# Kernel optimization log

Hardware: AMD Instinct MI355X
Metric: run time of the kernel (lower is better)

## Reference

```python
import jax, jax.numpy as jnp
import numpy as np

H = 1024
L = 2

def setup_inputs() -> dict:
    key = jax.random.key(0)
    k1, k2, k3, k4, k5 = jax.random.split(key, 5)
    B, S = 32, 2048
    scale = 1.0 / np.sqrt(H)
    return {
        "query": jax.random.normal(k1, (B, 1, H * L), dtype=jnp.float32),
        "keys": jax.random.normal(k2, (B, S, H), dtype=jnp.float32),
        "Wa_w": jax.random.normal(k3, (H * L, H), dtype=jnp.float32) * scale,
        "Wa_b": jnp.zeros((H,), dtype=jnp.float32),
        "Ua_w": jax.random.normal(k4, (H, H), dtype=jnp.float32) * scale,
        "Ua_b": jnp.zeros((H,), dtype=jnp.float32),
        "Va_w": jax.random.normal(k5, (H, 1), dtype=jnp.float32) * scale,
        "Va_b": jnp.zeros((1,), dtype=jnp.float32),
    }

def reference(query, keys, Wa_w, Wa_b, Ua_w, Ua_b, Va_w, Va_b):
    # query: [B,1,H*L], keys: [B,S,H]
    q = jnp.einsum('bqd,dh->bqh', query, Wa_w) + Wa_b   # [B,1,H]
    k = jnp.einsum('bsd,dh->bsh', keys, Ua_w) + Ua_b    # [B,S,H]
    e = jnp.tanh(q + k)                                  # [B,S,H]
    scores = jnp.einsum('bsh,ho->bso', e, Va_w) + Va_b   # [B,S,1]
    scores = scores[:, :, 0][:, None, :]                 # [B,1,S]
    weights = jax.nn.softmax(scores, axis=-1)            # [B,1,S]
    context = jnp.einsum('bqs,bsh->bqh', weights, keys)  # [B,1,H]
    return (context, weights)
```

## Files before the change

kernel.cpp:

```cpp
#include <hip/hip_runtime.h>
#include <hip/hip_bf16.h>


typedef __attribute__((ext_vector_type(8))) short short8;
typedef __attribute__((ext_vector_type(4))) float floatx4;

typedef const __attribute__((address_space(1))) unsigned int gu32;
typedef __attribute__((address_space(3))) unsigned int lu32;

__device__ __forceinline__ unsigned short f2bf(float f) {
    union { float f; unsigned int u; } c; c.f = f;
    unsigned int u = c.u + 0x7fffu + ((c.u >> 16) & 1u);
    return (unsigned short)(u >> 16);
}

__device__ __forceinline__ unsigned int f2bf2(float lo, float hi) {
#if __has_builtin(__builtin_amdgcn_cvt_pk_bf16_f32)
    auto r = __builtin_amdgcn_cvt_pk_bf16_f32(lo, hi);
    unsigned int u; __builtin_memcpy(&u, &r, 4);
    return u;
#else
    return (unsigned int)f2bf(lo) | ((unsigned int)f2bf(hi) << 16);
#endif
}

__device__ __forceinline__ void gld16(const unsigned short* g, unsigned short* l) {
    __builtin_amdgcn_global_load_lds(
        (gu32*)(uintptr_t)g,
        (lu32*)(unsigned int)(uintptr_t)l,
        16, 0, 0);
}

__global__ __launch_bounds__(256) void qproj_k(
    const float* __restrict__ query, const float* __restrict__ Wa,
    const float* __restrict__ Wab, const float* __restrict__ Uab,
    float* __restrict__ qws)
{
    __shared__ float qs[2048];
    __shared__ float red[16*64];
    const int tid = threadIdx.x;
    const int b = blockIdx.x, hc = blockIdx.y;
    #pragma unroll
    for (int i = 0; i < 8; i++) qs[tid + 256*i] = query[b*2048 + tid + 256*i];
    __syncthreads();
    const int hq = tid & 15;
    const int dg = tid >> 4;
    const float4* wp = reinterpret_cast<const float4*>(Wa + (size_t)(dg*128)*1024 + hc*64 + hq*4);
    const float* qp = qs + dg*128;
    float4 a0; a0.x = a0.y = a0.z = a0.w = 0.f;
    float4 a1; a1.x = a1.y = a1.z = a1.w = 0.f;
    #pragma unroll 4
    for (int d = 0; d < 128; d += 2) {
        float q0 = qp[d], q1 = qp[d+1];
        float4 w0 = wp[(size_t)d*256];
        float4 w1 = wp[(size_t)(d+1)*256];
        a0.x += q0*w0.x; a0.y += q0*w0.y; a0.z += q0*w0.z; a0.w += q0*w0.w;
        a1.x += q1*w1.x; a1.y += q1*w1.y; a1.z += q1*w1.z; a1.w += q1*w1.w;
    }
    a0.x += a1.x; a0.y += a1.y; a0.z += a1.z; a0.w += a1.w;
    *reinterpret_cast<float4*>(red + dg*64 + hq*4) = a0;
    __syncthreads();
    if (tid < 64) {
        float v = 0.f;
        #pragma unroll
        for (int g = 0; g < 16; g++) v += red[g*64 + tid];
        int hh = hc*64 + tid;
        qws[b*1024 + hh] = v + Wab[hh] + Uab[hh];
    }
}

__global__ __launch_bounds__(256) void uat_k(const float* __restrict__ Ua,
                                             unsigned short* __restrict__ uat)
{
    __shared__ unsigned short t[64][65];
    const int x = threadIdx.x & 63, yy = threadIdx.x >> 6;
    const int d0 = blockIdx.x*64, h0 = blockIdx.y*64;
    #pragma unroll
    for (int i = 0; i < 16; i++) {
        int y = yy*16 + i;
        t[y][x] = f2bf(Ua[(size_t)(d0+y)*1024 + h0 + x]);
    }
    __syncthreads();
    #pragma unroll
    for (int i = 0; i < 16; i++) {
        int y = yy*16 + i;
        uat[(size_t)(h0+y)*1024 + d0 + x] = t[x][y];
    }
}

__global__ __launch_bounds__(256) void kb16_k(const float* __restrict__ keys,
                                              unsigned short* __restrict__ kb,
                                              unsigned int nf4)
{
    const unsigned int stride = gridDim.x * 256u;
    unsigned int f = blockIdx.x * 256u + threadIdx.x;
    #pragma unroll 4
    for (int it = 0; it < 4; ++it, f += stride) {
        if (f < nf4) {
            unsigned int elem = f << 2;
            unsigned int rg   = elem >> 10;
            unsigned int rem  = elem & 1023u;
            unsigned int g    = rem >> 5;
            unsigned int c    = (rem >> 3) & 3u;
            unsigned int half = (rem >> 2) & 1u;
            unsigned int p    = ((rg & 2047u) >> 1) & 3u;
            float4 v = reinterpret_cast<const float4*>(keys)[f];
            uint2 w;
            w.x = f2bf2(v.x, v.y);
            w.y = f2bf2(v.z, v.w);
            unsigned int dst = rg*1024u + g*32u + ((c ^ p) << 3) + (half << 2);
            *reinterpret_cast<uint2*>(kb + dst) = w;
        }
    }
}

__global__ __launch_bounds__(256) void score_gemm_fast(
    const unsigned short* __restrict__ kb16,
    const unsigned short* __restrict__ uat,
    const float* __restrict__ qws,
    const float* __restrict__ Va,
    float* __restrict__ score,
    int b0)
{
    __shared__ unsigned short aS[2][128*32];
    __shared__ unsigned short bS[2][128*32];
    const int tid = threadIdx.x;
    const int bz = blockIdx.z;
    const int b = b0 + bz;
    const int s0 = blockIdx.x * 128;
    const int h0 = blockIdx.y * 128;
    const int lane = tid & 63, wave = tid >> 6;
    const int quad = lane >> 4, l15 = lane & 15;
    const int wm = (wave & 1) * 64, wn = (wave >> 1) * 64;

    const int srow = lane >> 2;
    const int schunk = (lane & 3) ^ ((srow >> 1) & 3);
    const int c0 = wave*2, c1 = wave*2 + 1;
    const unsigned short* ubase = uat + (size_t)h0*1024;
    const size_t boff0 = (size_t)(c0*16 + srow)*1024 + schunk*8;
    const size_t boff1 = (size_t)(c1*16 + srow)*1024 + schunk*8;

    const unsigned short* kA = kb16 + (size_t)(bz*2048 + s0)*1024;
    const size_t aoff0 = (size_t)(tid >> 2)*1024 + (size_t)(tid & 3)*8;
    const size_t aoff1 = (size_t)(64 + (tid >> 2))*1024 + (size_t)(tid & 3)*8;

    floatx4 acc[4][4];
    #pragma unroll
    for (int i = 0; i < 4; i++)
        #pragma unroll
        for (int j = 0; j < 4; j++) acc[i][j] = (floatx4)0.0f;

    gld16(kA + aoff0,    aS[0] + wave*512);
    gld16(kA + aoff1,    aS[0] + 2048 + wave*512);
    gld16(ubase + boff0, bS[0] + c0*512);
    gld16(ubase + boff1, bS[0] + c1*512);
    __syncthreads();

    int cur = 0;
    for (int kt = 0; kt < 31; ++kt) {
        const int nxt = cur ^ 1;
        const int k1 = (kt + 1) << 5;

        gld16(kA + aoff0 + k1,    aS[nxt] + wave*512);
        gld16(kA + aoff1 + k1,    aS[nxt] + 2048 + wave*512);
        gld16(ubase + boff0 + k1, bS[nxt] + c0*512);
        gld16(ubase + boff1 + k1, bS[nxt] + c1*512);

        short8 af[4], bf8[4];
        #pragma unroll
        for (int i = 0; i < 4; i++) {
            int row = wm + 16*i + l15;
            af[i] = *reinterpret_cast<const short8*>(aS[cur] + row*32 + ((quad ^ ((row>>1)&3)) * 8));
        }
        #pragma unroll
        for (int j = 0; j < 4; j++) {
            int row = wn + 16*j + l15;
            bf8[j] = *reinterpret_cast<const short8*>(bS[cur] + row*32 + ((quad ^ ((row>>1)&3)) * 8));
        }
        #pragma unroll
        for (int i = 0; i < 4; i++)
            #pragma unroll
            for (int j = 0; j < 4; j++)
                acc[i][j] = __builtin_amdgcn_mfma_f32_16x16x32_bf16(af[i], bf8[j], acc[i][j], 0, 0, 0);

        __syncthreads();
        cur = nxt;
    }

    {
        short8 af[4], bf8[4];
        #pragma unroll
        for (int i = 0; i < 4; i++) {
            int row = wm + 16*i + l15;
            af[i] = *reinterpret_cast<const short8*>(aS[cur] + row*32 + ((quad ^ ((row>>1)&3)) * 8));
        }
        #pragma unroll
        for (int j = 0; j < 4; j++) {
            int row = wn + 16*j + l15;
            bf8[j] = *reinterpret_cast<const short8*>(bS[cur] + row*32 + ((quad ^ ((row>>1)&3)) * 8));
        }
        #pragma unroll
        for (int i = 0; i < 4; i++)
            #pragma unroll
            for (int j = 0; j < 4; j++)
                acc[i][j] = __builtin_amdgcn_mfma_f32_16x16x32_bf16(af[i], bf8[j], acc[i][j], 0, 0, 0);
    }

    float qv[4], vav[4];
    #pragma unroll
    for (int j = 0; j < 4; j++) {
        int n = h0 + wn + 16*j + l15;
        qv[j]  = qws[b*1024 + n];
        vav[j] = Va[n];
    }
    #pragma unroll
    for (int i = 0; i < 4; i++) {
        #pragma unroll
        for (int r = 0; r < 4; r++) {
            float p = 0.f;
            #pragma unroll
            for (int j = 0; j < 4; j++) {
                float x = qv[j] + acc[i][j][r];
                float e = __expf(2.f * x);
                float t = 1.f - 2.f * __builtin_amdgcn_rcpf(e + 1.f);
                p += vav[j] * t;
            }
            #pragma unroll
            for (int off = 1; off < 16; off <<= 1) p += __shfl_xor(p, off, 64);
            if (l15 == 0) {
                int m = wm + 16*i + quad*4 + r;
                atomicAdd(score + (size_t)b*2048 + s0 + m, p);
            }
        }
    }
}

__global__ __launch_bounds__(256) void softmax_k(const float* __restrict__ score,
                                                 float* __restrict__ out_w)
{
    const int tid = threadIdx.x;
    const int b = blockIdx.x;
    __shared__ float wred[4], wred2[4];
    float sc[8];
    float mx = -3.0e38f;
    #pragma unroll
    for (int i = 0; i < 8; i++) {
        sc[i] = score[(size_t)b*2048 + tid + 256*i];
        mx = fmaxf(mx, sc[i]);
    }
    #pragma unroll
    for (int off = 32; off >= 1; off >>= 1) mx = fmaxf(mx, __shfl_xor(mx, off, 64));
    if ((tid & 63) == 0) wred[tid >> 6] = mx;
    __syncthreads();
    mx = fmaxf(fmaxf(wred[0], wred[1]), fmaxf(wred[2], wred[3]));
    float e[8]; float lsum = 0.f;
    #pragma unroll
    for (int i = 0; i < 8; i++) { e[i] = __expf(sc[i] - mx); lsum += e[i]; }
    #pragma unroll
    for (int off = 32; off >= 1; off >>= 1) lsum += __shfl_xor(lsum, off, 64);
    if ((tid & 63) == 0) wred2[tid >> 6] = lsum;
    __syncthreads();
    float inv = 1.0f / (wred2[0] + wred2[1] + wred2[2] + wred2[3]);
    #pragma unroll
    for (int i = 0; i < 8; i++) out_w[b*2048 + tid + 256*i] = e[i] * inv;
}

__global__ __launch_bounds__(256) void ctx_k(const float* __restrict__ keys,
                                             const float* __restrict__ w,
                                             float* __restrict__ ctxp, int sper)
{
    const int tid = threadIdx.x;
    const int b = blockIdx.x, sc = blockIdx.y;
    const float4* k4 = reinterpret_cast<const float4*>(keys) + (size_t)(b*2048 + sc*sper)*256;
    const float* wp = w + b*2048 + sc*sper;
    float4 a; a.x = a.y = a.z = a.w = 0.f;
    #pragma unroll 4
    for (int s = 0; s < sper; s++) {
        float wv = wp[s];
        float4 kv = k4[(size_t)s*256 + tid];
        a.x += wv*kv.x; a.y += wv*kv.y; a.z += wv*kv.z; a.w += wv*kv.w;
    }
    reinterpret_cast<float4*>(ctxp)[((size_t)b*gridDim.y + sc)*256 + tid] = a;
}

__global__ __launch_bounds__(256) void ctxsum_k(const float* __restrict__ ctxp,
                                                float* __restrict__ out, int nc)
{
    const int idx = blockIdx.x*256 + threadIdx.x;
    const int b = idx >> 10, h = idx & 1023;
    float v = 0.f;
    for (int s = 0; s < nc; s++) v += ctxp[((size_t)b*nc + s)*1024 + h];
    out[idx] = v;
}

extern "C" void kernel_launch(void* const* d_in, const int* in_sizes, int n_in,
                              void* d_out, int out_size, void* d_ws, size_t ws_size,
                              hipStream_t stream)
{
    const float* query = (const float*)d_in[0];
    const float* keys  = (const float*)d_in[1];
    const float* Wa_w  = (const float*)d_in[2];
    const float* Wa_b  = (const float*)d_in[3];
    const float* Ua_w  = (const float*)d_in[4];
    const float* Ua_b  = (const float*)d_in[5];
    const float* Va_w  = (const float*)d_in[6];

    char* ws = (char*)d_ws;
    float*          qws     = (float*)(ws);
    unsigned short* uat     = (unsigned short*)(ws + (131072));
    float*          score   = (float*)(ws + (131072 + 2097152));
    float*          ctxp    = (float*)(ws + (131072 + 2097152 + 4194304));
    const size_t BASE = 131072 + 2097152 + 4194304 + 2097152;
    unsigned short* kb16 = (unsigned short*)(ws + BASE);

    size_t avail = (ws_size > BASE) ? (ws_size - BASE) : 0;
    int nb = 32;
    while (nb > 1 && (size_t)nb * 2048 * 1024 * 2 > avail) nb >>= 1;

    float* out_ctx = (float*)d_out;
    float* out_w   = out_ctx + 32*1024;

    hipMemsetAsync(score, 0, 32*2048*sizeof(float), stream);
    qproj_k<<<dim3(32, 16), 256, 0, stream>>>(query, Wa_w, Wa_b, Ua_b, qws);
    uat_k  <<<dim3(16, 16), 256, 0, stream>>>(Ua_w, uat);
    for (int b0 = 0; b0 < 32; b0 += nb) {
        unsigned int nf4 = (unsigned int)nb * 2048u * 256u;
        unsigned int nthr = (nf4 + 3u) / 4u;
        unsigned int nblk = (nthr + 255u) / 256u;
        kb16_k<<<dim3(nblk), 256, 0, stream>>>(keys + (size_t)b0*2048*1024, kb16, nf4);
        score_gemm_fast<<<dim3(16, 8, nb), 256, 0, stream>>>(kb16, uat, qws, Va_w, score, b0);
    }
    softmax_k<<<dim3(32),      256, 0, stream>>>(score, out_w);
    ctx_k    <<<dim3(32, 16),  256, 0, stream>>>(keys, out_w, ctxp, 128);
    ctxsum_k <<<dim3(128),     256, 0, stream>>>(ctxp, out_ctx, 16);
}
```

Before: 647.4 us.

## Widen score GEMM tile to 128x256 and fuse context reduction via atomics

The score GEMM block tile grows from 128x128 to 128x256 along H. Each wave now computes 64x128 with 32 accumulators, which halves the B-tile loads and the atomic score writes per output and improves reuse of the A tile in LDS. Separately, the context partial-sum kernel is removed, and ctx_k atomically adds its partials straight into the zeroed output. The trade-offs are higher register pressure (128 accumulator floats per thread), more LDS, half as many blocks (lower occupancy and parallelism), and nondeterministic float atomics.

New measurement: 622.4 us. 3.9% less time.

```diff
diff --git a/kernel.cpp b/kernel.cpp
--- a/kernel.cpp
+++ b/kernel.cpp
@@ -123,37 +123,41 @@
     int b0)
 {
     __shared__ unsigned short aS[2][128*32];
-    __shared__ unsigned short bS[2][128*32];
+    __shared__ unsigned short bS[2][256*32];
     const int tid = threadIdx.x;
     const int bz = blockIdx.z;
     const int b = b0 + bz;
     const int s0 = blockIdx.x * 128;
-    const int h0 = blockIdx.y * 128;
+    const int h0 = blockIdx.y * 256;
     const int lane = tid & 63, wave = tid >> 6;
     const int quad = lane >> 4, l15 = lane & 15;
-    const int wm = (wave & 1) * 64, wn = (wave >> 1) * 64;
+    const int wm = (wave & 1) * 64, wn = (wave >> 1) * 128;
 
     const int srow = lane >> 2;
     const int schunk = (lane & 3) ^ ((srow >> 1) & 3);
-    const int c0 = wave*2, c1 = wave*2 + 1;
     const unsigned short* ubase = uat + (size_t)h0*1024;
-    const size_t boff0 = (size_t)(c0*16 + srow)*1024 + schunk*8;
-    const size_t boff1 = (size_t)(c1*16 + srow)*1024 + schunk*8;
+    size_t boff[4];
+    #pragma unroll
+    for (int u = 0; u < 4; u++) {
+        int cg = wave*4 + u;
+        boff[u] = (size_t)(cg*16 + srow)*1024 + schunk*8;
+    }
 
     const unsigned short* kA = kb16 + (size_t)(bz*2048 + s0)*1024;
     const size_t aoff0 = (size_t)(tid >> 2)*1024 + (size_t)(tid & 3)*8;
     const size_t aoff1 = (size_t)(64 + (tid >> 2))*1024 + (size_t)(tid & 3)*8;
 
-    floatx4 acc[4][4];
+    floatx4 acc[4][8];
     #pragma unroll
     for (int i = 0; i < 4; i++)
         #pragma unroll
-        for (int j = 0; j < 4; j++) acc[i][j] = (floatx4)0.0f;
-
-    gld16(kA + aoff0,    aS[0] + wave*512);
-    gld16(kA + aoff1,    aS[0] + 2048 + wave*512);
-    gld16(ubase + boff0, bS[0] + c0*512);
-    gld16(ubase + boff1, bS[0] + c1*512);
+        for (int j = 0; j < 8; j++) acc[i][j] = (floatx4)0.0f;
+
+    gld16(kA + aoff0, aS[0] + wave*512);
+    gld16(kA + aoff1, aS[0] + 2048 + wave*512);
+    #pragma unroll
+    for (int u = 0; u < 4; u++)
+        gld16(ubase + boff[u], bS[0] + (wave*4 + u)*512);
     __syncthreads();
 
     int cur = 0;
@@ -161,26 +165,27 @@
         const int nxt = cur ^ 1;
         const int k1 = (kt + 1) << 5;
 
-        gld16(kA + aoff0 + k1,    aS[nxt] + wave*512);
-        gld16(kA + aoff1 + k1,    aS[nxt] + 2048 + wave*512);
-        gld16(ubase + boff0 + k1, bS[nxt] + c0*512);
-        gld16(ubase + boff1 + k1, bS[nxt] + c1*512);
-
-        short8 af[4], bf8[4];
+        gld16(kA + aoff0 + k1, aS[nxt] + wave*512);
+        gld16(kA + aoff1 + k1, aS[nxt] + 2048 + wave*512);
+        #pragma unroll
+        for (int u = 0; u < 4; u++)
+            gld16(ubase + boff[u] + k1, bS[nxt] + (wave*4 + u)*512);
+
+        short8 af[4], bf8[8];
         #pragma unroll
         for (int i = 0; i < 4; i++) {
             int row = wm + 16*i + l15;
             af[i] = *reinterpret_cast<const short8*>(aS[cur] + row*32 + ((quad ^ ((row>>1)&3)) * 8));
         }
         #pragma unroll
-        for (int j = 0; j < 4; j++) {
+        for (int j = 0; j < 8; j++) {
             int row = wn + 16*j + l15;
             bf8[j] = *reinterpret_cast<const short8*>(bS[cur] + row*32 + ((quad ^ ((row>>1)&3)) * 8));
         }
         #pragma unroll
         for (int i = 0; i < 4; i++)
             #pragma unroll
-            for (int j = 0; j < 4; j++)
+            for (int j = 0; j < 8; j++)
                 acc[i][j] = __builtin_amdgcn_mfma_f32_16x16x32_bf16(af[i], bf8[j], acc[i][j], 0, 0, 0);
 
         __syncthreads();
@@ -188,27 +193,27 @@
     }
 
     {
-        short8 af[4], bf8[4];
+        short8 af[4], bf8[8];
         #pragma unroll
         for (int i = 0; i < 4; i++) {
             int row = wm + 16*i + l15;
             af[i] = *reinterpret_cast<const short8*>(aS[cur] + row*32 + ((quad ^ ((row>>1)&3)) * 8));
         }
         #pragma unroll
-        for (int j = 0; j < 4; j++) {
+        for (int j = 0; j < 8; j++) {
             int row = wn + 16*j + l15;
             bf8[j] = *reinterpret_cast<const short8*>(bS[cur] + row*32 + ((quad ^ ((row>>1)&3)) * 8));
         }
         #pragma unroll
         for (int i = 0; i < 4; i++)
             #pragma unroll
-            for (int j = 0; j < 4; j++)
+            for (int j = 0; j < 8; j++)
                 acc[i][j] = __builtin_amdgcn_mfma_f32_16x16x32_bf16(af[i], bf8[j], acc[i][j], 0, 0, 0);
     }
 
-    float qv[4], vav[4];
-    #pragma unroll
-    for (int j = 0; j < 4; j++) {
+    float qv[8], vav[8];
+    #pragma unroll
+    for (int j = 0; j < 8; j++) {
         int n = h0 + wn + 16*j + l15;
         qv[j]  = qws[b*1024 + n];
         vav[j] = Va[n];
@@ -219,7 +224,7 @@
         for (int r = 0; r < 4; r++) {
             float p = 0.f;
             #pragma unroll
-            for (int j = 0; j < 4; j++) {
+            for (int j = 0; j < 8; j++) {
                 float x = qv[j] + acc[i][j][r];
                 float e = __expf(2.f * x);
                 float t = 1.f - 2.f * __builtin_amdgcn_rcpf(e + 1.f);
@@ -267,7 +272,7 @@
 
 __global__ __launch_bounds__(256) void ctx_k(const float* __restrict__ keys,
                                              const float* __restrict__ w,
-                                             float* __restrict__ ctxp, int sper)
+                                             float* __restrict__ out_ctx, int sper)
 {
     const int tid = threadIdx.x;
     const int b = blockIdx.x, sc = blockIdx.y;
@@ -280,17 +285,11 @@
         float4 kv = k4[(size_t)s*256 + tid];
         a.x += wv*kv.x; a.y += wv*kv.y; a.z += wv*kv.z; a.w += wv*kv.w;
     }
-    reinterpret_cast<float4*>(ctxp)[((size_t)b*gridDim.y + sc)*256 + tid] = a;
-}
-
-__global__ __launch_bounds__(256) void ctxsum_k(const float* __restrict__ ctxp,
-                                                float* __restrict__ out, int nc)
-{
-    const int idx = blockIdx.x*256 + threadIdx.x;
-    const int b = idx >> 10, h = idx & 1023;
-    float v = 0.f;
-    for (int s = 0; s < nc; s++) v += ctxp[((size_t)b*nc + s)*1024 + h];
-    out[idx] = v;
+    float* o = out_ctx + (size_t)b*1024 + tid*4;
+    atomicAdd(o + 0, a.x);
+    atomicAdd(o + 1, a.y);
+    atomicAdd(o + 2, a.z);
+    atomicAdd(o + 3, a.w);
 }
 
 extern "C" void kernel_launch(void* const* d_in, const int* in_sizes, int n_in,
@@ -309,7 +308,6 @@
     float*          qws     = (float*)(ws);
     unsigned short* uat     = (unsigned short*)(ws + (131072));
     float*          score   = (float*)(ws + (131072 + 2097152));
-    float*          ctxp    = (float*)(ws + (131072 + 2097152 + 4194304));
     const size_t BASE = 131072 + 2097152 + 4194304 + 2097152;
     unsigned short* kb16 = (unsigned short*)(ws + BASE);
 
@@ -321,6 +319,7 @@
     float* out_w   = out_ctx + 32*1024;
 
     hipMemsetAsync(score, 0, 32*2048*sizeof(float), stream);
+    hipMemsetAsync(out_ctx, 0, 32*1024*sizeof(float), stream);
     qproj_k<<<dim3(32, 16), 256, 0, stream>>>(query, Wa_w, Wa_b, Ua_b, qws);
     uat_k  <<<dim3(16, 16), 256, 0, stream>>>(Ua_w, uat);
     for (int b0 = 0; b0 < 32; b0 += nb) {
@@ -328,9 +327,8 @@
         unsigned int nthr = (nf4 + 3u) / 4u;
         unsigned int nblk = (nthr + 255u) / 256u;
         kb16_k<<<dim3(nblk), 256, 0, stream>>>(keys + (size_t)b0*2048*1024, kb16, nf4);
-        score_gemm_fast<<<dim3(16, 8, nb), 256, 0, stream>>>(kb16, uat, qws, Va_w, score, b0);
+        score_gemm_fast<<<dim3(16, 4, nb), 256, 0, stream>>>(kb16, uat, qws, Va_w, score, b0);
     }
     softmax_k<<<dim3(32),      256, 0, stream>>>(score, out_w);
-    ctx_k    <<<dim3(32, 16),  256, 0, stream>>>(keys, out_w, ctxp, 128);
-    ctxsum_k <<<dim3(128),     256, 0, stream>>>(ctxp, out_ctx, 16);
-}
+    ctx_k    <<<dim3(32, 16),  256, 0, stream>>>(keys, out_w, out_ctx, 128);
+}
```
